# Kernel optimization log

Hardware: AMD Instinct MI355X
Metric: run time of the kernel (lower is better)

The kernel has to match this reference:

```python
import jax, jax.numpy as jnp
import numpy as np

V = 20000   # input_size (POI vocab)
U = 10000   # user_count
H = 128     # hidden_size
B = 64      # user_len (batch)
S = 200     # seq_len
LAM_T = 0.01
LAM_S = 100.0
DAY = 86400.0


def setup_inputs() -> dict:
    key = jax.random.key(0)
    ks = jax.random.split(key, 12)
    sc = 1.0 / np.sqrt(H)
    return {
        "poi_inputs": jax.random.randint(ks[0], (B, S), 0, V),
        "lengths": jnp.full((B,), S, dtype=jnp.int32),  # full sequences -> pack/pad is identity
        "timestamp_inputs": jnp.sort(jax.random.uniform(ks[1], (B, S), minval=0.0, maxval=DAY), axis=1),
        "location_inputs": jax.random.normal(ks[2], (B, S, 2)) * 0.1,
        "active_user": jax.random.randint(ks[3], (B,), 0, U),
        "emb_W": jax.random.normal(ks[4], (V, H)),      # nn.Embedding default N(0,1)
        "user_W": jax.random.normal(ks[5], (U, H)),
        "W_ih": jax.random.uniform(ks[6], (H, H), minval=-sc, maxval=sc),
        "W_hh": jax.random.uniform(ks[7], (H, H), minval=-sc, maxval=sc),
        "b_ih": jax.random.uniform(ks[8], (H,), minval=-sc, maxval=sc),
        "b_hh": jax.random.uniform(ks[9], (H,), minval=-sc, maxval=sc),
        "fc_W": jax.random.uniform(ks[10], (V, 2 * H), minval=-sc, maxval=sc),  # torch Linear [out,in]
        "fc_b": jax.random.uniform(ks[11], (V,), minval=-sc, maxval=sc),
    }


def _safe_norm(d):
    # norm over last axis with zero (not nan) gradient at d == 0
    d2 = jnp.sum(d * d, axis=-1)
    pos = d2 > 0
    return jnp.where(pos, jnp.sqrt(jnp.where(pos, d2, 1.0)), 0.0)


def reference(poi_inputs, lengths, timestamp_inputs, location_inputs, active_user,
              emb_W, user_W, W_ih, W_hh, b_ih, b_hh, fc_W, fc_b):
    t, s = timestamp_inputs, location_inputs
    x_emb = emb_W[poi_inputs]                       # [B,S,H]

    # vanilla tanh RNN (torch nn.RNN, batch_first) via scan over time
    def step(h, xt):
        h = jnp.tanh(xt @ W_ih.T + b_ih + h @ W_hh.T + b_hh)
        return h, h
    h0 = jnp.zeros((x_emb.shape[0], W_hh.shape[0]), x_emb.dtype)
    _, out = jax.lax.scan(step, h0, jnp.swapaxes(x_emb, 0, 1))
    out = jnp.swapaxes(out, 0, 1)                   # [B,S,H]

    # vectorized spatio-temporal decay attention (original O(S^2) python loop)
    dt = jnp.maximum(t[:, :, None] - t[:, None, :], 0.0)          # [B,S,S] clamp_min(0)
    ds = _safe_norm(s[:, :, None, :] - s[:, None, :, :])          # [B,S,S]
    a_j = ((jnp.cos(dt * (2.0 * jnp.pi / DAY)) + 1.0) * 0.5) * jnp.exp(-dt * LAM_T)
    b_j = jnp.exp(-ds * LAM_S)
    causal = jnp.tril(jnp.ones((t.shape[1], t.shape[1]), bool))   # j <= i
    w = jnp.where(causal, a_j * b_j + 1e-10, 0.0)                 # [B,S,S]
    sum_w = jnp.maximum(jnp.sum(w, axis=-1), 1e-10)               # [B,S]
    out_w = jnp.einsum('bij,bjh->bih', w, out) / sum_w[..., None] # [B,S,H]

    p_u = jnp.broadcast_to(user_W[active_user][:, None, :], out_w.shape)
    out_pu = jnp.concatenate([out_w, p_u], axis=-1)               # [B,S,2H]
    y = jax.nn.softmax(out_pu @ fc_W.T + fc_b, axis=-1)           # [B,S,V]
    return y, out_pu
```

## Files before the change

### kernel.cpp

```cpp
#include <hip/hip_runtime.h>
#include <hip/hip_bf16.h>
#include <stdint.h>

#define B_   64
#define S_   200
#define H_   128
#define V_   20000
#define M_   12800
#define NPAD 20224
#define NBN  158
#define NBM  100
#define NWG2 15800

#define WS_A      0u
#define WS_FCW    3276800u
#define WS_U      8454144u
#define WS_RSUM   13631488u
#define WS_WTIH   13682688u

#define XP_OFF    0
#define HOUT_OFF  2000000
#define PART_OFF  4000000
#define OUTPU_OFF 256000000ll

typedef __attribute__((ext_vector_type(8))) __bf16 bf16x8;
typedef __attribute__((ext_vector_type(4))) float  f32x4;

__device__ __forceinline__ void gll16(const void* g, void* l) {
  __builtin_amdgcn_global_load_lds(
      (const __attribute__((address_space(1))) void*)g,
      (__attribute__((address_space(3))) void*)l, 16, 0, 0);
}

__global__ __launch_bounds__(256)
void prep_w1(const float* __restrict__ fcw, __hip_bfloat16* __restrict__ w1) {
  int t = threadIdx.x;
  int row = blockIdx.x * 2 + (t >> 7);
  int col = t & 127;
  float v = (row < V_) ? fcw[(long)row * 256 + col] : 0.f;
  w1[(long)row * 128 + col] = __float2bfloat16(v);
}

__global__ __launch_bounds__(128)
void prep_wt(const float* __restrict__ w_ih, float* __restrict__ wt) {
  int bid = blockIdx.x, t = threadIdx.x;
  wt[bid * 128 + t] = w_ih[t * 128 + bid];
}

__global__ __launch_bounds__(256)
void user_k(const int* __restrict__ auser, const float* __restrict__ userW,
            const float* __restrict__ fcW, const float* __restrict__ fcb,
            float* __restrict__ U) {
  __shared__ float uw[8][128];
  int t = threadIdx.x;
  int c = blockIdx.x * 256 + t;
  int b0 = blockIdx.y * 8;
  for (int i = t; i < 8 * 128; i += 256) {
    int bb = i >> 7, kk = i & 127;
    uw[bb][kk] = userW[(long)auser[b0 + bb] * 128 + kk];
  }
  __syncthreads();
  float acc[8];
#pragma unroll
  for (int bb = 0; bb < 8; ++bb) acc[bb] = 0.f;
  if (c < V_) {
    const float* w2 = fcW + (long)c * 256 + 128;
#pragma unroll 4
    for (int k = 0; k < 128; k += 4) {
      float4 wv = *(const float4*)(w2 + k);
#pragma unroll
      for (int bb = 0; bb < 8; ++bb) {
        acc[bb] = fmaf(wv.x, uw[bb][k], acc[bb]);
        acc[bb] = fmaf(wv.y, uw[bb][k + 1], acc[bb]);
        acc[bb] = fmaf(wv.z, uw[bb][k + 2], acc[bb]);
        acc[bb] = fmaf(wv.w, uw[bb][k + 3], acc[bb]);
      }
    }
    float base = fcb[c];
#pragma unroll
    for (int bb = 0; bb < 8; ++bb)
      U[(long)(b0 + bb) * NPAD + c] = base + acc[bb];
  } else {
#pragma unroll
    for (int bb = 0; bb < 8; ++bb)
      U[(long)(b0 + bb) * NPAD + c] = -1e30f;
  }
}

__global__ __launch_bounds__(128)
void xproj_k(const int* __restrict__ poi, const float* __restrict__ emb,
             const float* __restrict__ wt_ih, const float* __restrict__ b_ih,
             const float* __restrict__ b_hh, float* __restrict__ xp) {
  __shared__ float xs[16][128];
  int j = threadIdx.x;
  int m0 = blockIdx.x * 16;
#pragma unroll
  for (int i = 0; i < 16; ++i)
    xs[i][j] = emb[(long)poi[m0 + i] * 128 + j];
  __syncthreads();
  float bias = b_ih[j] + b_hh[j];
  float acc[16];
#pragma unroll
  for (int i = 0; i < 16; ++i) acc[i] = bias;
  for (int kq = 0; kq < 32; ++kq) {
    float w0 = wt_ih[(4 * kq + 0) * 128 + j];
    float w1 = wt_ih[(4 * kq + 1) * 128 + j];
    float w2 = wt_ih[(4 * kq + 2) * 128 + j];
    float w3 = wt_ih[(4 * kq + 3) * 128 + j];
#pragma unroll
    for (int i = 0; i < 16; ++i) {
      float4 xv = *(const float4*)&xs[i][4 * kq];
      acc[i] = fmaf(xv.x, w0, acc[i]);
      acc[i] = fmaf(xv.y, w1, acc[i]);
      acc[i] = fmaf(xv.z, w2, acc[i]);
      acc[i] = fmaf(xv.w, w3, acc[i]);
    }
  }
#pragma unroll
  for (int i = 0; i < 16; ++i)
    xp[(long)(m0 + i) * 128 + j] = acc[i];
}

__global__ __launch_bounds__(128)
void rnn_k(const float* __restrict__ xp, const float* __restrict__ w_hh,
           float* __restrict__ hout) {
  int b = blockIdx.x, j = threadIdx.x;
  float w[128];
#pragma unroll
  for (int k = 0; k < 128; ++k) w[k] = w_hh[j * 128 + k];
  __shared__ float hs[2][128];
  hs[0][j] = 0.f;
  __syncthreads();
  int cur = 0;
  for (int t = 0; t < S_; ++t) {
    float x0 = xp[((long)b * S_ + t) * 128 + j];
    const float4* hp4 = (const float4*)hs[cur];
    float a0 = 0.f, a1 = 0.f, a2 = 0.f, a3 = 0.f;
#pragma unroll
    for (int k = 0; k < 8; ++k) {
      float4 v0 = hp4[k], v1 = hp4[k + 8], v2 = hp4[k + 16], v3 = hp4[k + 24];
      a0 = fmaf(v0.x, w[4 * k + 0], a0); a0 = fmaf(v0.y, w[4 * k + 1], a0);
      a0 = fmaf(v0.z, w[4 * k + 2], a0); a0 = fmaf(v0.w, w[4 * k + 3], a0);
      a1 = fmaf(v1.x, w[32 + 4 * k + 0], a1); a1 = fmaf(v1.y, w[32 + 4 * k + 1], a1);
      a1 = fmaf(v1.z, w[32 + 4 * k + 2], a1); a1 = fmaf(v1.w, w[32 + 4 * k + 3], a1);
      a2 = fmaf(v2.x, w[64 + 4 * k + 0], a2); a2 = fmaf(v2.y, w[64 + 4 * k + 1], a2);
      a2 = fmaf(v2.z, w[64 + 4 * k + 2], a2); a2 = fmaf(v2.w, w[64 + 4 * k + 3], a2);
      a3 = fmaf(v3.x, w[96 + 4 * k + 0], a3); a3 = fmaf(v3.y, w[96 + 4 * k + 1], a3);
      a3 = fmaf(v3.z, w[96 + 4 * k + 2], a3); a3 = fmaf(v3.w, w[96 + 4 * k + 3], a3);
    }
    float hn = tanhf(x0 + ((a0 + a1) + (a2 + a3)));
    hs[cur ^ 1][j] = hn;
    hout[((long)b * S_ + t) * 128 + j] = hn;
    cur ^= 1;
    __syncthreads();
  }
}

__global__ __launch_bounds__(128)
void attn_k(const float* __restrict__ ts, const float* __restrict__ loc,
            const float* __restrict__ hout, const int* __restrict__ auser,
            const float* __restrict__ userW, float* __restrict__ outpu,
            __hip_bfloat16* __restrict__ Abf) {
  int i = blockIdx.x, b = blockIdx.y, h = threadIdx.x;
  __shared__ float wl[128];
  const float OMEGA = 7.27220521664304e-05f;
  float ti = ts[b * S_ + i];
  float lx = loc[(b * S_ + i) * 2 + 0];
  float ly = loc[(b * S_ + i) * 2 + 1];
  float acc = 0.f, sw = 0.f;
  for (int jc = 0; jc <= i; jc += 128) {
    int j = jc + h;
    float wj = 0.f;
    if (j <= i) {
      float dt = fmaxf(ti - ts[b * S_ + j], 0.f);
      float a = (cosf(dt * OMEGA) + 1.f) * 0.5f * expf(-dt * 0.01f);
      float dx = lx - loc[(b * S_ + j) * 2 + 0];
      float dy = ly - loc[(b * S_ + j) * 2 + 1];
      float dn = sqrtf(dx * dx + dy * dy);
      wj = a * expf(-dn * 100.f) + 1e-10f;
    }
    __syncthreads();
    wl[h] = wj;
    __syncthreads();
    int lim = min(128, i - jc + 1);
    const float* hb = hout + ((long)b * S_ + jc) * 128 + h;
    for (int jj = 0; jj < lim; ++jj) {
      float wv = wl[jj];
      acc = fmaf(wv, hb[(long)jj * 128], acc);
      sw += wv;
    }
  }
  float ow = acc / fmaxf(sw, 1e-10f);
  long m = (long)b * S_ + i;
  float pu = userW[(long)auser[b] * 128 + h];
  outpu[m * 256 + h]       = ow;
  outpu[m * 256 + 128 + h] = pu;
  Abf[m * 128 + h]         = __float2bfloat16(ow);
}

template <int PASS>
__global__ __launch_bounds__(512, 4)
void gemm_fc(const __hip_bfloat16* __restrict__ A,
             const __hip_bfloat16* __restrict__ Bw,
             const float* __restrict__ Ut,
             const float* __restrict__ rowsum,
             float* __restrict__ part,
             float* __restrict__ y) {
  __shared__ __align__(16) char smem[65536];
  __shared__ float rsum4[4][128];
  char* AsB = smem;
  char* BsB = smem + 32768;
  float* lbuf = (float*)smem;

  const int tid  = threadIdx.x;
  const int lane = tid & 63;
  const int wid  = tid >> 6;
  const int wr = wid >> 2, wc = wid & 3;
  const int g = lane >> 4, lr = lane & 15;

  const int orig = blockIdx.x;
  const int nid = (orig & 7) * (NWG2 / 8) + (orig >> 3);
  const int bn = nid / NBM, bm = nid % NBM;
  const long brow = (long)bm * 128, bcol = (long)bn * 128;

  const char* Ab = (const char*)A + brow * 256;
  const char* Bb = (const char*)Bw + bcol * 256;

#pragma unroll
  for (int i = 0; i < 4; ++i) {
    int ci = i * 512 + tid;
    int row = ci >> 4;
    int w = (ci & 15) ^ (row & 7);
    long src = (long)row * 256 + (long)w * 16;
    gll16(Ab + src, AsB + (long)ci * 16);
    gll16(Bb + src, BsB + (long)ci * 16);
  }
  __syncthreads();

  f32x4 acc[4][2];
#pragma unroll
  for (int mi = 0; mi < 4; ++mi)
#pragma unroll
    for (int ni = 0; ni < 2; ++ni) acc[mi][ni] = (f32x4)(0.f);

#pragma unroll
  for (int kk = 0; kk < 4; ++kk) {
    bf16x8 af[4], bfr[2];
#pragma unroll
    for (int mi = 0; mi < 4; ++mi) {
      int row = wr * 64 + mi * 16 + lr;
      int w = ((kk << 2) | g) ^ (row & 7);
      af[mi] = *(const bf16x8*)(AsB + row * 256 + w * 16);
    }
#pragma unroll
    for (int ni = 0; ni < 2; ++ni) {
      int row = wc * 32 + ni * 16 + lr;
      int w = ((kk << 2) | g) ^ (row & 7);
      bfr[ni] = *(const bf16x8*)(BsB + row * 256 + w * 16);
    }
#pragma unroll
    for (int mi = 0; mi < 4; ++mi)
#pragma unroll
      for (int ni = 0; ni < 2; ++ni)
        acc[mi][ni] = __builtin_amdgcn_mfma_f32_16x16x32_bf16(af[mi], bfr[ni], acc[mi][ni], 0, 0, 0);
  }

  if (PASS == 0) {
#pragma unroll
    for (int mi = 0; mi < 4; ++mi) {
#pragma unroll
      for (int r = 0; r < 4; ++r) {
        long row = brow + wr * 64 + mi * 16 + g * 4 + r;
        const float* urow = Ut + (long)(row / S_) * NPAD + bcol;
        float s = 0.f;
#pragma unroll
        for (int ni = 0; ni < 2; ++ni) {
          float u = urow[wc * 32 + ni * 16 + lr];
          s += __expf(acc[mi][ni][r] + u);
        }
#pragma unroll
        for (int off = 1; off < 16; off <<= 1) s += __shfl_xor(s, off);
        if (lr == 0) rsum4[wc][wr * 64 + mi * 16 + g * 4 + r] = s;
      }
    }
    __syncthreads();
    if (tid < 128)
      part[(long)bn * M_ + brow + tid] =
          rsum4[0][tid] + rsum4[1][tid] + rsum4[2][tid] + rsum4[3][tid];
  } else {
    if (bcol >= V_) return;
    const bool full = (bcol + 128 <= V_);
    __syncthreads();
#pragma unroll
    for (int mi = 0; mi < 4; ++mi) {
#pragma unroll
      for (int r = 0; r < 4; ++r) {
        int lrow = wr * 64 + mi * 16 + g * 4 + r;
        long row = brow + lrow;
        const float* urow = Ut + (long)(row / S_) * NPAD + bcol;
        float inv = 1.0f / rowsum[row];
        int key = ((lrow >> 2) & 3) << 2;
#pragma unroll
        for (int ni = 0; ni < 2; ++ni) {
          int lcol = wc * 32 + ni * 16 + lr;
          lbuf[lrow * 128 + (lcol ^ key)] = __expf(acc[mi][ni][r] + urow[lcol]) * inv;
        }
      }
    }
    __syncthreads();
    if (full) {
#pragma unroll
      for (int it = 0; it < 8; ++it) {
        int idx = it * 512 + tid;
        int lrow = idx >> 5, c4 = idx & 31;
        int key = ((lrow >> 2) & 3) << 2;
        f32x4 v = *(const f32x4*)(lbuf + lrow * 128 + ((c4 * 4) ^ key));
        __builtin_nontemporal_store(v,
            (f32x4*)(y + (brow + lrow) * (long)V_ + bcol + c4 * 4));
      }
    } else {
#pragma unroll
      for (int it = 0; it < 8; ++it) {
        int idx = it * 512 + tid;
        int lrow = idx >> 5, c4 = idx & 31;
        int key = ((lrow >> 2) & 3) << 2;
        const float* src = lbuf + lrow * 128 + ((c4 * 4) ^ key);
        long row = brow + lrow;
#pragma unroll
        for (int e = 0; e < 4; ++e) {
          int col = (int)bcol + c4 * 4 + e;
          if (col < V_) y[row * (long)V_ + col] = src[e];
        }
      }
    }
  }
}

__global__ void reduce_rows(const float* __restrict__ part, float* __restrict__ rowsum) {
  int m = blockIdx.x * 256 + threadIdx.x;
  if (m < M_) {
    float s = 0.f;
    for (int bn = 0; bn < NBN; ++bn) s += part[(long)bn * M_ + m];
    rowsum[m] = fmaxf(s, 1e-30f);
  }
}

extern "C" void kernel_launch(void* const* d_in, const int* in_sizes, int n_in,
                              void* d_out, int out_size, void* d_ws, size_t ws_size,
                              hipStream_t stream) {
  const int*   poi   = (const int*)d_in[0];
  const float* ts    = (const float*)d_in[2];
  const float* loc   = (const float*)d_in[3];
  const int*   auser = (const int*)d_in[4];
  const float* embW  = (const float*)d_in[5];
  const float* userW = (const float*)d_in[6];
  const float* w_ih  = (const float*)d_in[7];
  const float* w_hh  = (const float*)d_in[8];
  const float* b_ih  = (const float*)d_in[9];
  const float* b_hh  = (const float*)d_in[10];
  const float* fcW   = (const float*)d_in[11];
  const float* fcb   = (const float*)d_in[12];

  float* out = (float*)d_out;
  char*  ws  = (char*)d_ws;
  __hip_bfloat16* Abf    = (__hip_bfloat16*)(ws + WS_A);
  __hip_bfloat16* w1b    = (__hip_bfloat16*)(ws + WS_FCW);
  float*          Ut     = (float*)(ws + WS_U);
  float*          rowsum = (float*)(ws + WS_RSUM);
  float*          wt_ih  = (float*)(ws + WS_WTIH);

  float* xp    = out + XP_OFF;
  float* hout  = out + HOUT_OFF;
  float* part  = out + PART_OFF;
  float* outpu = out + OUTPU_OFF;

  prep_w1<<<dim3(NPAD / 2), dim3(256), 0, stream>>>(fcW, w1b);
  prep_wt<<<dim3(128), dim3(128), 0, stream>>>(w_ih, wt_ih);
  user_k<<<dim3(NPAD / 256, 8), dim3(256), 0, stream>>>(auser, userW, fcW, fcb, Ut);
  xproj_k<<<dim3(M_ / 16), dim3(128), 0, stream>>>(poi, embW, wt_ih, b_ih, b_hh, xp);
  rnn_k<<<dim3(B_), dim3(128), 0, stream>>>(xp, w_hh, hout);
  attn_k<<<dim3(S_, B_), dim3(128), 0, stream>>>(ts, loc, hout, auser, userW, outpu, Abf);
  gemm_fc<0><<<dim3(NWG2), dim3(512), 0, stream>>>(Abf, w1b, Ut, nullptr, part, nullptr);
  reduce_rows<<<dim3(50), dim3(256), 0, stream>>>(part, rowsum);
  gemm_fc<1><<<dim3(NWG2), dim3(512), 0, stream>>>(Abf, w1b, Ut, rowsum, nullptr, out);
}
```

Measured before the change: 737.2 us.

## Vectorize LDS reads in user/attention kernels and swap GEMM tile ordering

```diff
diff --git a/kernel.cpp b/kernel.cpp
--- a/kernel.cpp
+++ b/kernel.cpp
@@ -65,15 +65,15 @@
   for (int bb = 0; bb < 8; ++bb) acc[bb] = 0.f;
   if (c < V_) {
     const float* w2 = fcW + (long)c * 256 + 128;
-#pragma unroll 4
-    for (int k = 0; k < 128; k += 4) {
-      float4 wv = *(const float4*)(w2 + k);
+    for (int kq = 0; kq < 32; ++kq) {
+      float4 wv = *(const float4*)(w2 + 4 * kq);
 #pragma unroll
       for (int bb = 0; bb < 8; ++bb) {
-        acc[bb] = fmaf(wv.x, uw[bb][k], acc[bb]);
-        acc[bb] = fmaf(wv.y, uw[bb][k + 1], acc[bb]);
-        acc[bb] = fmaf(wv.z, uw[bb][k + 2], acc[bb]);
-        acc[bb] = fmaf(wv.w, uw[bb][k + 3], acc[bb]);
+        float4 uv = *(const float4*)&uw[bb][4 * kq];
+        acc[bb] = fmaf(wv.x, uv.x, acc[bb]);
+        acc[bb] = fmaf(wv.y, uv.y, acc[bb]);
+        acc[bb] = fmaf(wv.z, uv.z, acc[bb]);
+        acc[bb] = fmaf(wv.w, uv.w, acc[bb]);
       }
     }
     float base = fcb[c];
@@ -184,7 +184,19 @@
     __syncthreads();
     int lim = min(128, i - jc + 1);
     const float* hb = hout + ((long)b * S_ + jc) * 128 + h;
-    for (int jj = 0; jj < lim; ++jj) {
+    int jj = 0;
+    for (; jj + 4 <= lim; jj += 4) {
+      float4 wv4 = *(const float4*)&wl[jj];
+      float h0 = hb[(long)(jj + 0) * 128];
+      float h1 = hb[(long)(jj + 1) * 128];
+      float h2 = hb[(long)(jj + 2) * 128];
+      float h3 = hb[(long)(jj + 3) * 128];
+      acc = fmaf(wv4.x, h0, acc); sw += wv4.x;
+      acc = fmaf(wv4.y, h1, acc); sw += wv4.y;
+      acc = fmaf(wv4.z, h2, acc); sw += wv4.z;
+      acc = fmaf(wv4.w, h3, acc); sw += wv4.w;
+    }
+    for (; jj < lim; ++jj) {
       float wv = wl[jj];
       acc = fmaf(wv, hb[(long)jj * 128], acc);
       sw += wv;
@@ -220,7 +232,7 @@
 
   const int orig = blockIdx.x;
   const int nid = (orig & 7) * (NWG2 / 8) + (orig >> 3);
-  const int bn = nid / NBM, bm = nid % NBM;
+  const int bm = nid / NBN, bn = nid % NBN;
   const long brow = (long)bm * 128, bcol = (long)bn * 128;
 
   const char* Ab = (const char*)A + brow * 256;
```

New measurement: 762.6 us. +3.4%, slower.
